# Performance work log

Measured on AMD Instinct MI355X. Metric: run time of the kernel, lower is better.

## Reference

```python
import jax, jax.numpy as jnp
import numpy as np

B, N, C, H, F = 4, 256, 256, 8, 64  # batch, nodes, in_channels, heads, n_hidden


def setup_inputs() -> dict:
    key = jax.random.key(0)
    k1, k2, k3, k4, k5 = jax.random.split(key, 5)
    x = jax.random.normal(k1, (B, N, C), jnp.float32)
    W_l = jax.random.normal(k2, (C, H * F), jnp.float32) / np.sqrt(C)
    W_r = jax.random.normal(k3, (C, H * F), jnp.float32) / np.sqrt(C)
    attn_w = jax.random.normal(k4, (F,), jnp.float32) / np.sqrt(F)
    adj = jax.random.randint(k5, (N, N, H), 0, 2, jnp.int32)
    # guarantee at least one unmasked head per (i, j) pair so the
    # softmax-over-heads (dim=-1 in the source) never sees all -inf
    adj = adj.at[:, :, 0].set(1)
    return {"x": x, "W_l": W_l, "W_r": W_r, "attn_w": attn_w, "adj": adj}


def reference(x, W_l, W_r, attn_w, adj):
    b, n, _ = x.shape
    g_l = (x @ W_l).reshape(b, n, H, F)
    g_r = (x @ W_r).reshape(b, n, H, F)
    # torch: g_l.repeat(1,n,1,1) + g_r.repeat_interleave(n,dim=1), then
    # view(b,n,n,h,f)  =>  g_sum[b,i,j,h,f] = g_r[b,i] + g_l[b,j]
    g_sum = g_r[:, :, None] + g_l[:, None, :]          # [b,i,j,h,f]
    e = jnp.einsum('bijhf,f->bijh', jax.nn.leaky_relu(g_sum, 0.2), attn_w)
    e = jnp.where(adj == 0, -jnp.inf, e)               # adj broadcasts over batch
    a = jax.nn.softmax(e, axis=-1)                     # softmax over heads, per source (dim=-1)
    out = jnp.einsum('bijh,bjhf->bihf', a, g_r)        # aggregate over neighbors j
    return out.reshape(b, n, H * F)                    # is_concat=True
```

## Files before the change

### kernel.cpp

```cpp
#include <hip/hip_runtime.h>
#include <hip/hip_bf16.h>

constexpr int kB = 4, kN = 256, kC = 256, kH = 8, kF = 64, kHF = 512;

__device__ __forceinline__ float2 bf2_unpack(unsigned int u) {
    union { unsigned int i; float f; } a, b;
    a.i = u << 16;
    b.i = u & 0xffff0000u;
    return make_float2(a.f, b.f);
}

__device__ __forceinline__ void unpack8(uint4 p, float* o) {
    float2 v0 = bf2_unpack(p.x), v1 = bf2_unpack(p.y);
    float2 v2 = bf2_unpack(p.z), v3 = bf2_unpack(p.w);
    o[0] = v0.x; o[1] = v0.y; o[2] = v1.x; o[3] = v1.y;
    o[4] = v2.x; o[5] = v2.y; o[6] = v3.x; o[7] = v3.y;
}

__device__ __forceinline__ unsigned short f2bf(float f) {
    union { float f; unsigned int i; } v; v.f = f;
    unsigned int r = v.i + 0x7fffu + ((v.i >> 16) & 1u);
    return (unsigned short)(r >> 16);
}

__global__ __launch_bounds__(256) void gat_gemm_kernel(
    const float* __restrict__ x,
    const float* __restrict__ Wl,
    const float* __restrict__ Wr,
    unsigned short* __restrict__ gl,
    unsigned short* __restrict__ gr)
{
    __shared__ float xs[8][kC];
    const int rowBase = blockIdx.x * 8;
    const float* Wm = (blockIdx.y == 0) ? Wl : Wr;
    unsigned short* gout = (blockIdx.y == 0) ? gl : gr;

    const int tid = threadIdx.x;

    {
        const int r = tid >> 5;
        const int kc = (tid & 31) * 8;
        const float* xp = x + (rowBase + r) * kC + kc;
        float4 v0 = *(const float4*)xp;
        float4 v1 = *(const float4*)(xp + 4);
        *(float4*)&xs[r][kc]     = v0;
        *(float4*)&xs[r][kc + 4] = v1;
    }
    __syncthreads();

    const int c0 = tid * 2;
    float acc[8][2];
#pragma unroll
    for (int r = 0; r < 8; ++r) { acc[r][0] = 0.f; acc[r][1] = 0.f; }

    for (int k = 0; k < kC; k += 4) {
        float2 wv[4];
#pragma unroll
        for (int kk = 0; kk < 4; ++kk)
            wv[kk] = *(const float2*)(Wm + (k + kk) * kHF + c0);
#pragma unroll
        for (int r = 0; r < 8; ++r) {
            float4 xv = *(const float4*)&xs[r][k];
            acc[r][0] = fmaf(xv.x, wv[0].x, acc[r][0]);
            acc[r][1] = fmaf(xv.x, wv[0].y, acc[r][1]);
            acc[r][0] = fmaf(xv.y, wv[1].x, acc[r][0]);
            acc[r][1] = fmaf(xv.y, wv[1].y, acc[r][1]);
            acc[r][0] = fmaf(xv.z, wv[2].x, acc[r][0]);
            acc[r][1] = fmaf(xv.z, wv[2].y, acc[r][1]);
            acc[r][0] = fmaf(xv.w, wv[3].x, acc[r][0]);
            acc[r][1] = fmaf(xv.w, wv[3].y, acc[r][1]);
        }
    }

#pragma unroll
    for (int r = 0; r < 8; ++r) {
        unsigned int p = (unsigned int)f2bf(acc[r][0]) |
                         ((unsigned int)f2bf(acc[r][1]) << 16);
        ((unsigned int*)gout)[(((rowBase + r) * kHF) + c0) >> 1] = p;
    }
}

__global__ __launch_bounds__(512) void gat_attn_kernel(
    const unsigned short* __restrict__ gl,
    const unsigned short* __restrict__ gr,
    const float* __restrict__ attn_w,
    const int* __restrict__ adj,
    float* __restrict__ out)
{
    __shared__ float red[8 * kHF];

    const int bi = blockIdx.x;
    const int b = bi >> 8;
    const int i = bi & 255;
    const int tid = threadIdx.x;
    const int wv = tid >> 6;
    const int lane = tid & 63;
    const int h = lane >> 3;
    const int fg = lane & 7;
    const int fbase = fg * 8;

    float gri[8], wf[8];
    {
        uint4 pk = *(const uint4*)(gr + (size_t)bi * kHF + h * kF + fbase);
        unpack8(pk, gri);
        float4 wa = *(const float4*)(attn_w + fbase);
        float4 wb = *(const float4*)(attn_w + fbase + 4);
        wf[0] = wa.x; wf[1] = wa.y; wf[2] = wa.z; wf[3] = wa.w;
        wf[4] = wb.x; wf[5] = wb.y; wf[6] = wb.z; wf[7] = wb.w;
    }

    float acc[8];
#pragma unroll
    for (int k = 0; k < 8; ++k) acc[k] = 0.f;

    const int adjbase = i * kN * kH;
    const size_t gbase = (size_t)(b * kN) * kHF + h * kF + fbase;

    for (int j = wv; j < kN; j += 8) {
        uint4 glk = *(const uint4*)(gl + gbase + (size_t)j * kHF);
        uint4 grk = *(const uint4*)(gr + gbase + (size_t)j * kHF);
        float glv[8], grv[8];
        unpack8(glk, glv);
        unpack8(grk, grv);

        float e = 0.f;
#pragma unroll
        for (int k = 0; k < 8; ++k) {
            float s = gri[k] + glv[k];
            float u = fmaf(0.4f, fabsf(s), 0.6f * s);
            e = fmaf(u, wf[k], e);
        }
        e += __shfl_xor(e, 1);
        e += __shfl_xor(e, 2);
        e += __shfl_xor(e, 4);

        int av = adj[adjbase + j * kH + h];
        e = av ? e : -1e30f;

        float m = e;
        m = fmaxf(m, __shfl_xor(m, 8));
        m = fmaxf(m, __shfl_xor(m, 16));
        m = fmaxf(m, __shfl_xor(m, 32));
        float ex = __expf(e - m);
        float den = ex;
        den += __shfl_xor(den, 8);
        den += __shfl_xor(den, 16);
        den += __shfl_xor(den, 32);
        float a = ex / den;

#pragma unroll
        for (int k = 0; k < 8; ++k) acc[k] = fmaf(a, grv[k], acc[k]);
    }

    float* rp = &red[wv * kHF + lane * 8];
#pragma unroll
    for (int k = 0; k < 8; ++k) rp[k] = acc[k];
    __syncthreads();

    float s = 0.f;
#pragma unroll
    for (int w8 = 0; w8 < 8; ++w8) s += red[w8 * kHF + tid];

    out[(size_t)bi * kHF + tid] = s;
}

extern "C" void kernel_launch(void* const* d_in, const int* in_sizes, int n_in,
                              void* d_out, int out_size, void* d_ws, size_t ws_size,
                              hipStream_t stream) {
    const float* x  = (const float*)d_in[0];
    const float* Wl = (const float*)d_in[1];
    const float* Wr = (const float*)d_in[2];
    const float* aw = (const float*)d_in[3];
    const int* adj  = (const int*)d_in[4];

    unsigned short* gl = (unsigned short*)d_ws;
    unsigned short* gr = gl + (size_t)kB * kN * kHF;

    dim3 g1(kB * kN / 8, 2);
    gat_gemm_kernel<<<g1, 256, 0, stream>>>(x, Wl, Wr, gl, gr);

    gat_attn_kernel<<<kB * kN, 512, 0, stream>>>(
        gl, gr, aw, adj, (float*)d_out);
}
```

Measured before the change: 125.9 us.

## Process four target nodes per attention block with packed fp16 math

The attention kernel now handles four target rows i per block, so each loaded gl/gr row for neighbor j is reused across four nodes instead of being refetched. Intermediates switch from bf16 to fp16 so the score uses packed half adds, max-based leaky ReLU and fdot2. The softmax drops the max subtraction and uses a reciprocal instead of a divide. The GEMM is retiled to four rows per block. Risks: lower fp16 precision, overflow in an unguarded exp, fewer attention blocks, and more registers and shared memory per block.

```diff
diff --git a/kernel.cpp b/kernel.cpp
--- a/kernel.cpp
+++ b/kernel.cpp
@@ -1,57 +1,38 @@
 #include <hip/hip_runtime.h>
 #include <hip/hip_bf16.h>
 
+typedef _Float16 h2 __attribute__((ext_vector_type(2)));
+
 constexpr int kB = 4, kN = 256, kC = 256, kH = 8, kF = 64, kHF = 512;
+constexpr int kIPB = 4;
 
-__device__ __forceinline__ float2 bf2_unpack(unsigned int u) {
-    union { unsigned int i; float f; } a, b;
-    a.i = u << 16;
-    b.i = u & 0xffff0000u;
-    return make_float2(a.f, b.f);
-}
-
-__device__ __forceinline__ void unpack8(uint4 p, float* o) {
-    float2 v0 = bf2_unpack(p.x), v1 = bf2_unpack(p.y);
-    float2 v2 = bf2_unpack(p.z), v3 = bf2_unpack(p.w);
-    o[0] = v0.x; o[1] = v0.y; o[2] = v1.x; o[3] = v1.y;
-    o[4] = v2.x; o[5] = v2.y; o[6] = v3.x; o[7] = v3.y;
-}
-
-__device__ __forceinline__ unsigned short f2bf(float f) {
-    union { float f; unsigned int i; } v; v.f = f;
-    unsigned int r = v.i + 0x7fffu + ((v.i >> 16) & 1u);
-    return (unsigned short)(r >> 16);
-}
+union H2U { h2 h; unsigned int u; };
 
 __global__ __launch_bounds__(256) void gat_gemm_kernel(
     const float* __restrict__ x,
     const float* __restrict__ Wl,
     const float* __restrict__ Wr,
-    unsigned short* __restrict__ gl,
-    unsigned short* __restrict__ gr)
+    unsigned int* __restrict__ gl,
+    unsigned int* __restrict__ gr)
 {
-    __shared__ float xs[8][kC];
-    const int rowBase = blockIdx.x * 8;
+    __shared__ float xs[4][kC];
+    const int rowBase = blockIdx.x * 4;
     const float* Wm = (blockIdx.y == 0) ? Wl : Wr;
-    unsigned short* gout = (blockIdx.y == 0) ? gl : gr;
+    unsigned int* gout = (blockIdx.y == 0) ? gl : gr;
 
     const int tid = threadIdx.x;
 
     {
-        const int r = tid >> 5;
-        const int kc = (tid & 31) * 8;
-        const float* xp = x + (rowBase + r) * kC + kc;
-        float4 v0 = *(const float4*)xp;
-        float4 v1 = *(const float4*)(xp + 4);
-        *(float4*)&xs[r][kc]     = v0;
-        *(float4*)&xs[r][kc + 4] = v1;
+        const int r = tid >> 6;
+        const int kc = (tid & 63) * 4;
+        *(float4*)&xs[r][kc] = *(const float4*)(x + (rowBase + r) * kC + kc);
     }
     __syncthreads();
 
     const int c0 = tid * 2;
-    float acc[8][2];
+    float acc[4][2];
 #pragma unroll
-    for (int r = 0; r < 8; ++r) { acc[r][0] = 0.f; acc[r][1] = 0.f; }
+    for (int r = 0; r < 4; ++r) { acc[r][0] = 0.f; acc[r][1] = 0.f; }
 
     for (int k = 0; k < kC; k += 4) {
         float2 wv[4];
@@ -59,7 +40,7 @@
         for (int kk = 0; kk < 4; ++kk)
             wv[kk] = *(const float2*)(Wm + (k + kk) * kHF + c0);
 #pragma unroll
-        for (int r = 0; r < 8; ++r) {
+        for (int r = 0; r < 4; ++r) {
             float4 xv = *(const float4*)&xs[r][k];
             acc[r][0] = fmaf(xv.x, wv[0].x, acc[r][0]);
             acc[r][1] = fmaf(xv.x, wv[0].y, acc[r][1]);
@@ -73,25 +54,24 @@
     }
 
 #pragma unroll
-    for (int r = 0; r < 8; ++r) {
-        unsigned int p = (unsigned int)f2bf(acc[r][0]) |
-                         ((unsigned int)f2bf(acc[r][1]) << 16);
-        ((unsigned int*)gout)[(((rowBase + r) * kHF) + c0) >> 1] = p;
+    for (int r = 0; r < 4; ++r) {
+        H2U p; p.h = (h2){(_Float16)acc[r][0], (_Float16)acc[r][1]};
+        gout[((rowBase + r) * kHF + c0) >> 1] = p.u;
     }
 }
 
 __global__ __launch_bounds__(512) void gat_attn_kernel(
-    const unsigned short* __restrict__ gl,
-    const unsigned short* __restrict__ gr,
+    const unsigned int* __restrict__ gl,
+    const unsigned int* __restrict__ gr,
     const float* __restrict__ attn_w,
     const int* __restrict__ adj,
     float* __restrict__ out)
 {
-    __shared__ float red[8 * kHF];
+    __shared__ float red[8 * kIPB * kHF];
 
-    const int bi = blockIdx.x;
-    const int b = bi >> 8;
-    const int i = bi & 255;
+    const int bi0 = blockIdx.x * kIPB;
+    const int b = bi0 >> 8;
+    const int i0 = bi0 & 255;
     const int tid = threadIdx.x;
     const int wv = tid >> 6;
     const int lane = tid & 63;
@@ -99,69 +79,102 @@
     const int fg = lane & 7;
     const int fbase = fg * 8;
 
-    float gri[8], wf[8];
+    h2 gri[kIPB][4];
+#pragma unroll
+    for (int ii = 0; ii < kIPB; ++ii) {
+        uint4 pk = *(const uint4*)(gr +
+            (((size_t)(bi0 + ii) * kHF + h * kF + fbase) >> 1));
+        H2U a0, a1, a2, a3;
+        a0.u = pk.x; a1.u = pk.y; a2.u = pk.z; a3.u = pk.w;
+        gri[ii][0] = a0.h; gri[ii][1] = a1.h; gri[ii][2] = a2.h; gri[ii][3] = a3.h;
+    }
+    h2 w2[4];
     {
-        uint4 pk = *(const uint4*)(gr + (size_t)bi * kHF + h * kF + fbase);
-        unpack8(pk, gri);
         float4 wa = *(const float4*)(attn_w + fbase);
         float4 wb = *(const float4*)(attn_w + fbase + 4);
-        wf[0] = wa.x; wf[1] = wa.y; wf[2] = wa.z; wf[3] = wa.w;
-        wf[4] = wb.x; wf[5] = wb.y; wf[6] = wb.z; wf[7] = wb.w;
+        w2[0] = (h2){(_Float16)wa.x, (_Float16)wa.y};
+        w2[1] = (h2){(_Float16)wa.z, (_Float16)wa.w};
+        w2[2] = (h2){(_Float16)wb.x, (_Float16)wb.y};
+        w2[3] = (h2){(_Float16)wb.z, (_Float16)wb.w};
     }
 
-    float acc[8];
+    float acc[kIPB][8];
 #pragma unroll
-    for (int k = 0; k < 8; ++k) acc[k] = 0.f;
+    for (int ii = 0; ii < kIPB; ++ii)
+#pragma unroll
+        for (int q = 0; q < 8; ++q) acc[ii][q] = 0.f;
 
-    const int adjbase = i * kN * kH;
-    const size_t gbase = (size_t)(b * kN) * kHF + h * kF + fbase;
+    const h2 c02 = (h2){(_Float16)0.2f, (_Float16)0.2f};
+    const size_t gcolbase = (size_t)(b * kN) * kHF + h * kF + fbase;
+    const int adjbase = i0 * kN * kH + h;
 
     for (int j = wv; j < kN; j += 8) {
-        uint4 glk = *(const uint4*)(gl + gbase + (size_t)j * kHF);
-        uint4 grk = *(const uint4*)(gr + gbase + (size_t)j * kHF);
-        float glv[8], grv[8];
-        unpack8(glk, glv);
-        unpack8(grk, grv);
+        const size_t off = (gcolbase + (size_t)j * kHF) >> 1;
+        uint4 ga = *(const uint4*)(gl + off);
+        uint4 gb = *(const uint4*)(gr + off);
 
-        float e = 0.f;
+        int am[kIPB];
 #pragma unroll
-        for (int k = 0; k < 8; ++k) {
-            float s = gri[k] + glv[k];
-            float u = fmaf(0.4f, fabsf(s), 0.6f * s);
-            e = fmaf(u, wf[k], e);
+        for (int ii = 0; ii < kIPB; ++ii)
+            am[ii] = adj[adjbase + (ii * kN + j) * kH];
+
+        h2 gl2[4], gr2[4];
+        { H2U t; t.u = ga.x; gl2[0] = t.h; t.u = ga.y; gl2[1] = t.h;
+                 t.u = ga.z; gl2[2] = t.h; t.u = ga.w; gl2[3] = t.h;
+                 t.u = gb.x; gr2[0] = t.h; t.u = gb.y; gr2[1] = t.h;
+                 t.u = gb.z; gr2[2] = t.h; t.u = gb.w; gr2[3] = t.h; }
+
+        float grf[8];
+#pragma unroll
+        for (int q = 0; q < 4; ++q) {
+            grf[2 * q]     = (float)gr2[q].x;
+            grf[2 * q + 1] = (float)gr2[q].y;
         }
-        e += __shfl_xor(e, 1);
-        e += __shfl_xor(e, 2);
-        e += __shfl_xor(e, 4);
-
-        int av = adj[adjbase + j * kH + h];
-        e = av ? e : -1e30f;
-
-        float m = e;
-        m = fmaxf(m, __shfl_xor(m, 8));
-        m = fmaxf(m, __shfl_xor(m, 16));
-        m = fmaxf(m, __shfl_xor(m, 32));
-        float ex = __expf(e - m);
-        float den = ex;
-        den += __shfl_xor(den, 8);
-        den += __shfl_xor(den, 16);
-        den += __shfl_xor(den, 32);
-        float a = ex / den;
 
 #pragma unroll
-        for (int k = 0; k < 8; ++k) acc[k] = fmaf(a, grv[k], acc[k]);
+        for (int ii = 0; ii < kIPB; ++ii) {
+            float e = 0.f;
+#pragma unroll
+            for (int q = 0; q < 4; ++q) {
+                h2 s = gri[ii][q] + gl2[q];
+                h2 u = __builtin_elementwise_max(s, c02 * s);
+                e = __builtin_amdgcn_fdot2(u, w2[q], e, false);
+            }
+            e += __shfl_xor(e, 1);
+            e += __shfl_xor(e, 2);
+            e += __shfl_xor(e, 4);
+
+            e = am[ii] ? e : -1e30f;
+
+            float ex = __expf(e);
+            float den = ex;
+            den += __shfl_xor(den, 8);
+            den += __shfl_xor(den, 16);
+            den += __shfl_xor(den, 32);
+            float a = ex * __builtin_amdgcn_rcpf(den);
+
+#pragma unroll
+            for (int q = 0; q < 8; ++q)
+                acc[ii][q] = fmaf(a, grf[q], acc[ii][q]);
+        }
     }
 
-    float* rp = &red[wv * kHF + lane * 8];
 #pragma unroll
-    for (int k = 0; k < 8; ++k) rp[k] = acc[k];
+    for (int ii = 0; ii < kIPB; ++ii) {
+        float* rp = &red[(wv * kIPB + ii) * kHF + lane * 8];
+#pragma unroll
+        for (int q = 0; q < 8; ++q) rp[q] = acc[ii][q];
+    }
     __syncthreads();
 
-    float s = 0.f;
 #pragma unroll
-    for (int w8 = 0; w8 < 8; ++w8) s += red[w8 * kHF + tid];
-
-    out[(size_t)bi * kHF + tid] = s;
+    for (int ii = 0; ii < kIPB; ++ii) {
+        float s = 0.f;
+#pragma unroll
+        for (int w8 = 0; w8 < 8; ++w8)
+            s += red[(w8 * kIPB + ii) * kHF + tid];
+        out[(size_t)(bi0 + ii) * kHF + tid] = s;
+    }
 }
 
 extern "C" void kernel_launch(void* const* d_in, const int* in_sizes, int n_in,
@@ -173,12 +186,12 @@
     const float* aw = (const float*)d_in[3];
     const int* adj  = (const int*)d_in[4];
 
-    unsigned short* gl = (unsigned short*)d_ws;
-    unsigned short* gr = gl + (size_t)kB * kN * kHF;
+    unsigned int* gl = (unsigned int*)d_ws;
+    unsigned int* gr = gl + (size_t)kB * kN * kHF / 2;
 
-    dim3 g1(kB * kN / 8, 2);
+    dim3 g1(kB * kN / 4, 2);
     gat_gemm_kernel<<<g1, 256, 0, stream>>>(x, Wl, Wr, gl, gr);
 
-    gat_attn_kernel<<<kB * kN, 512, 0, stream>>>(
+    gat_attn_kernel<<<kB * kN / kIPB, 512, 0, stream>>>(
         gl, gr, aw, adj, (float*)d_out);
 }
```

Result: faster. 113.0 us (-10.3%).
